# Kernel optimization log

Hardware: AMD Instinct MI355X
Metric: run time of the kernel (lower is better)

Reference implementation:

```python
import jax, jax.numpy as jnp
import numpy as np
from jax.scipy.stats import norm

B, IN, H0, H1, OUT = 1024, 2048, 4096, 4096, 1000
EPS_CDF = 1e-5
DECAY = 0.01
NEG_SLOPE = 0.01  # LeakyReLU default slope


def setup_inputs() -> dict:
    key = jax.random.key(0)
    ks = iter(jax.random.split(key, 40))
    rn = lambda shp, s=1.0: s * jax.random.normal(next(ks), shp, dtype=jnp.float32)
    inp = {}
    inp['x'] = rn((B, IN))
    inp['z_w'] = rn((IN,), 0.02)
    for nm, (o, i) in zip(['0', '1', 'o'], [(H0, IN), (H1, H0), (OUT, H1)]):
        inp['w_mu' + nm] = rn((o, i), 0.02)
        inp['w_ls' + nm] = rn((o, i), 0.1) - 2.0  # log-sigma ~ -2 => sigma ~ 0.13
        inp['b_mu' + nm] = rn((o,), 0.02)
        inp['b_ls' + nm] = rn((o,), 0.1) - 2.0
        inp['eps_w' + nm] = rn((o, i))
        inp['eps_b' + nm] = rn((o,))
    inp['pfz0'] = jax.random.uniform(next(ks), (B, H0), dtype=jnp.float32)
    inp['pfz1'] = jax.random.uniform(next(ks), (B, H1), dtype=jnp.float32)
    inp['y'] = jax.random.randint(next(ks), (B,), 0, OUT, dtype=jnp.int32)
    inp['mz0'] = jax.random.randint(next(ks), (B, H0), 0, 2, dtype=jnp.int32)
    inp['mz1'] = jax.random.randint(next(ks), (B, H1), 0, 2, dtype=jnp.int32)
    inp['mask_mu0'] = jax.random.randint(next(ks), (H0,), 0, 2, dtype=jnp.int32)
    inp['mask_mu1'] = jax.random.randint(next(ks), (H1,), 0, 2, dtype=jnp.int32)
    inp['data_set_size'] = 60000
    return inp


def _bayes_layer(h, w_mu, w_ls, b_mu, b_ls, eps_w, eps_b, mz, mask_mu, pfz):
    sw = jnp.exp(w_ls)
    sb = jnp.exp(b_ls)
    w = w_mu + sw * eps_w          # reparameterized weight sample
    b = b_mu + sb * eps_b
    h = h @ w.T + b                # F.linear
    h = jnp.where(h >= 0, h, NEG_SLOPE * h)  # LeakyReLU
    mzf = mz.astype(h.dtype)
    m = mzf * mask_mu.astype(h.dtype)[None, :]   # [B, h]
    mult = m.shape[1] / (m.sum(1) + 1e-6)        # rescale multiplier per sample
    h = h * m * mult[:, None]
    # GFN forward-flow log-prob of the z-mask
    p = jnp.clip(pfz, 1e-6, 1.0 - 1e-6)
    flow = (mzf * jnp.log(p) + (1.0 - mzf) * jnp.log(1.0 - p)).sum()
    # Gaussian CDF likelihood of sampled weights/biases (finite-difference density)
    pw = norm.cdf(w + EPS_CDF, w_mu, sw) - norm.cdf(w - EPS_CDF, w_mu, sw)
    pb = norm.cdf(b + EPS_CDF, b_mu, sb) - norm.cdf(b - EPS_CDF, b_mu, sb)
    flow = flow + jnp.log(pw).sum() + jnp.log(pb).sum()
    return h, flow


def reference(x, z_w, w_mu0, w_ls0, b_mu0, b_ls0, eps_w0, eps_b0,
              w_mu1, w_ls1, b_mu1, b_ls1, eps_w1, eps_b1,
              w_muo, w_lso, b_muo, b_lso, eps_wo, eps_bo,
              pfz0, pfz1, y, mz0, mz1, mask_mu0, mask_mu1, data_set_size):
    loss = (x @ z_w).sum()  # total flow estimator Z
    h, f0 = _bayes_layer(x, w_mu0, w_ls0, b_mu0, b_ls0, eps_w0, eps_b0, mz0, mask_mu0, pfz0)
    loss = loss + f0
    h, f1 = _bayes_layer(h, w_mu1, w_ls1, b_mu1, b_ls1, eps_w1, eps_b1, mz1, mask_mu1, pfz1)
    loss = loss + f1
    # output BayesLinear (sampled)
    wo = w_muo + jnp.exp(w_lso) * eps_wo
    bo = b_muo + jnp.exp(b_lso) * eps_bo
    pred = h @ wo.T + bo  # [B, OUT]
    logp = jax.nn.log_softmax(pred, axis=-1)
    ce = -jnp.take_along_axis(logp, y[:, None].astype(jnp.int32), axis=1).mean()
    loss = loss + jnp.float32(data_set_size) * ce  # NLL
    wd = DECAY * ((w_mu0 ** 2).sum() + jnp.exp(w_ls0).sum()
                  + (w_mu1 ** 2).sum() + jnp.exp(w_ls1).sum())
    loss = (loss + wd) ** 2
    return pred, loss
```

## Files before the change

kernel.cpp:

```cpp
#include <hip/hip_runtime.h>
#include <math.h>

#define B_SZ 1024
#define IN_SZ 2048
#define H0_SZ 4096
#define H1_SZ 4096
#define OUT_SZ 1000

typedef _Float16 f16;
typedef __attribute__((ext_vector_type(4))) _Float16 f16x4;
typedef __attribute__((ext_vector_type(8))) _Float16 f16x8;
typedef __attribute__((ext_vector_type(4))) float f32x4;

#define OFF_N0     0ULL
#define OFF_N1     4ULL
#define OFF_MSUM0  256ULL
#define OFF_MSUM1  4352ULL
#define OFF_CPOS0  8448ULL
#define OFF_CPOS1  24832ULL
#define OFF_IDX0   41216ULL
#define OFF_IDX1   57600ULL
#define OFF_PXZ    73984ULL
#define OFF_PFL    82176ULL
#define OFF_PCE    98560ULL
#define OFF_PB     106752ULL
#define OFF_PW     107776ULL
#define OFF_BS0    370688ULL
#define OFF_BS1    387072ULL
#define OFF_BSO    403456ULL
#define OFF_XH     407552ULL
#define OFF_XL     4601856ULL
#define OFF_H0H    8796160ULL
#define OFF_H0L    17184768ULL
#define OFF_H1H    25573376ULL
#define OFF_H1L    33961984ULL
#define OFF_W0CH   42350592ULL
#define OFF_W0CL   59127808ULL
#define OFF_W1CH   75905024ULL
#define OFF_W1CL   109459456ULL
#define OFF_WOCH   143013888ULL
#define OFF_WOCL   151402496ULL
#define OFF_PART   159791104ULL

#define PSTRIDE_H  2560
#define PSTRIDE_O  1024

#define RB_W1   4096
#define RB_WO   5096
#define RB_W0   9192
#define RB_FL0  10216
#define RB_FL1  11240
#define RB_SX   11496
#define RB_B0   11512
#define RB_B1   11528
#define RB_BO   11532

__device__ __forceinline__ void gload_lds16(const void* g, void* l)
{
    __builtin_amdgcn_global_load_lds((const __attribute__((address_space(1))) void*)g,
                                     (__attribute__((address_space(3))) void*)l, 16, 0, 0);
}

__device__ __forceinline__ void reduce4_store(double v0, double v1, double v2, double v3,
                                              double* dst)
{
    __shared__ double sh[4][4];
    double v[4] = {v0, v1, v2, v3};
    int lane = threadIdx.x & 63, wid = threadIdx.x >> 6;
#pragma unroll
    for (int a = 0; a < 4; ++a) {
        double x = v[a];
#pragma unroll
        for (int o = 32; o > 0; o >>= 1) x += __shfl_down(x, o, 64);
        if (lane == 0) sh[a][wid] = x;
    }
    __syncthreads();
    if (threadIdx.x == 0) {
        dst[0] = sh[0][0] + sh[0][1] + sh[0][2] + sh[0][3];
        dst[1] = sh[1][0] + sh[1][1] + sh[1][2] + sh[1][3];
        dst[2] = sh[2][0] + sh[2][1] + sh[2][2] + sh[2][3];
        dst[3] = sh[3][0] + sh[3][1] + sh[3][2] + sh[3][3];
    }
}

__device__ __forceinline__ void reduce1_store(double v, double* dst)
{
    __shared__ double sh1[4];
    int lane = threadIdx.x & 63, wid = threadIdx.x >> 6;
#pragma unroll
    for (int o = 32; o > 0; o >>= 1) v += __shfl_down(v, o, 64);
    if (lane == 0) sh1[wid] = v;
    __syncthreads();
    if (threadIdx.x == 0) dst[0] = sh1[0] + sh1[1] + sh1[2] + sh1[3];
}

__global__ __launch_bounds__(1024) void idxbuild_kernel(
    const int* __restrict__ mask0, const int* __restrict__ mask1,
    int* __restrict__ cpos0, int* __restrict__ idx0, int* __restrict__ n0,
    int* __restrict__ cpos1, int* __restrict__ idx1, int* __restrict__ n1)
{
    __shared__ int sh[1024];
    const int t = threadIdx.x;
    const int pass = blockIdx.x;
    const int* mask = pass ? mask1 : mask0;
    int* cpos = pass ? cpos1 : cpos0;
    int* idx = pass ? idx1 : idx0;
    int* np = pass ? n1 : n0;
    int4 m = ((const int4*)mask)[t];
    int s = m.x + m.y + m.z + m.w;
    sh[t] = s;
    __syncthreads();
    for (int o = 1; o < 1024; o <<= 1) {
        int v = (t >= o) ? sh[t - o] : 0;
        __syncthreads();
        sh[t] += v;
        __syncthreads();
    }
    int run = sh[t] - s;
    int4 cp;
    cp.x = run; cp.y = run + m.x; cp.z = cp.y + m.y; cp.w = cp.z + m.z;
    ((int4*)cpos)[t] = cp;
    if (m.x) idx[cp.x] = 4 * t + 0;
    if (m.y) idx[cp.y] = 4 * t + 1;
    if (m.z) idx[cp.z] = 4 * t + 2;
    if (m.w) idx[cp.w] = 4 * t + 3;
    if (t == 1023) *np = sh[1023];
}


__device__ void role_splitx(int rb, const float4* x, const float4* zw,
                            f16x4* xh, f16x4* xl, double* pxz)
{
    const int n4 = B_SZ * IN_SZ / 4;
    double s = 0;
    int i = rb * 256 + threadIdx.x;
    const int stride = 256 * 256;
    for (; i < n4; i += stride) {
        float4 v = x[i];
        float4 z = zw[i & (IN_SZ / 4 - 1)];
        s += (double)((v.x * z.x + v.y * z.y) + (v.z * z.z + v.w * z.w));
        f16 h0 = (f16)v.x, h1 = (f16)v.y, h2 = (f16)v.z, h3 = (f16)v.w;
        f16x4 hv = {h0, h1, h2, h3};
        f16x4 lv = {(f16)(v.x - (float)h0), (f16)(v.y - (float)h1),
                    (f16)(v.z - (float)h2), (f16)(v.w - (float)h3)};
        xh[i] = hv; xl[i] = lv;
    }
    reduce1_store(s, pxz + rb);
}

__device__ void role_flow(int b, const int* mz, const float* pfz, const int* maskmu,
                          float* msum, double* pfl)
{
    const int4* m4 = (const int4*)(mz + (size_t)b * 4096);
    const float4* p4 = (const float4*)(pfz + (size_t)b * 4096);
    const int4* k4 = (const int4*)maskmu;
    int s = 0;
    double fl = 0;
    for (int i = threadIdx.x; i < 1024; i += 256) {
        int4 m = m4[i];
        float4 p = p4[i];
        int4 k = k4[i];
        s += m.x * k.x + m.y * k.y + m.z * k.z + m.w * k.w;
        float a0 = fminf(fmaxf(p.x, 1e-6f), 1.0f - 1e-6f);
        float a1 = fminf(fmaxf(p.y, 1e-6f), 1.0f - 1e-6f);
        float a2 = fminf(fmaxf(p.z, 1e-6f), 1.0f - 1e-6f);
        float a3 = fminf(fmaxf(p.w, 1e-6f), 1.0f - 1e-6f);
        float g0 = logf(m.x ? a0 : 1.0f - a0);
        float g1 = logf(m.y ? a1 : 1.0f - a1);
        float g2 = logf(m.z ? a2 : 1.0f - a2);
        float g3 = logf(m.w ? a3 : 1.0f - a3);
        fl += (double)((g0 + g1) + (g2 + g3));
    }
#pragma unroll
    for (int o = 32; o > 0; o >>= 1) {
        s += __shfl_down(s, o, 64);
        fl += __shfl_down(fl, o, 64);
    }
    __shared__ int shi[4];
    __shared__ double shd[4];
    if ((threadIdx.x & 63) == 0) { shi[threadIdx.x >> 6] = s; shd[threadIdx.x >> 6] = fl; }
    __syncthreads();
    if (threadIdx.x == 0) {
        msum[b] = (float)(shi[0] + shi[1] + shi[2] + shi[3]);
        pfl[b] = shd[0] + shd[1] + shd[2] + shd[3];
    }
}

template <int RED>
__device__ void role_bsample(int rb, const float* bmu, const float* bls, const float* beps,
                             float* out, int n, double* pb)
{
    int i = rb * 256 + threadIdx.x;
    float l = 0.f, e = 0.f;
    if (i < n) {
        l = bls[i]; e = beps[i];
        out[i] = fmaf(__expf(l), e, bmu[i]);
    }
    if (RED) {
        double sls = (i < n) ? (double)l : 0.0;
        double se2 = (i < n) ? (double)e * e : 0.0;
        reduce4_store(sls, se2, 0.0, 0.0, pb + (size_t)rb * 4);
    }
}

__device__ void role_w0(int r, const float* mu, const float* ls, const float* eps,
                        const int* maskR, const int* cposR, f16* hi, double* pw)
{
    const size_t rbb = (size_t)r * IN_SZ;
    const float4* m4 = (const float4*)(mu + rbb);
    const float4* l4 = (const float4*)(ls + rbb);
    const float4* e4 = (const float4*)(eps + rbb);
    const bool wr_ = maskR[r] != 0;
    const int drow = cposR[r];
    f16* hrow = hi + (size_t)drow * IN_SZ;
    double sls = 0, se2 = 0, smu2 = 0, sex = 0;
    for (int i = threadIdx.x; i < IN_SZ / 4; i += 256) {
        float4 m = m4[i], l = l4[i], e = e4[i];
        float g0 = __expf(l.x), g1 = __expf(l.y), g2 = __expf(l.z), g3 = __expf(l.w);
        float w0 = fmaf(g0, e.x, m.x), w1 = fmaf(g1, e.y, m.y);
        float w2 = fmaf(g2, e.z, m.z), w3 = fmaf(g3, e.w, m.w);
        sls += (double)((l.x + l.y) + (l.z + l.w));
        se2 += (double)((e.x * e.x + e.y * e.y) + (e.z * e.z + e.w * e.w));
        smu2 += (double)((m.x * m.x + m.y * m.y) + (m.z * m.z + m.w * m.w));
        sex += (double)((g0 + g1) + (g2 + g3));
        if (wr_) {
            f16x4 hv = {(f16)w0, (f16)w1, (f16)w2, (f16)w3};
            *(f16x4*)(hrow + i * 4) = hv;
        }
    }
    reduce4_store(sls, se2, smu2, sex, pw + (size_t)r * 4);
}

__shared__ __align__(16) f16 g_ldsH[4096];

template <int ROWC, int RED>
__device__ void role_colc(int r, const float* mu, const float* ls, const float* eps,
                          const int* maskR, const int* cposR,
                          const int* maskC, const int* cposC, const int* pNc,
                          f16* hi, double* pw)
{
    const size_t rbb = (size_t)r * 4096;
    const float4* m4 = (const float4*)(mu + rbb);
    const float4* l4 = (const float4*)(ls + rbb);
    const float4* e4 = (const float4*)(eps + rbb);
    const bool wr_ = ROWC ? (maskR[r] != 0) : true;
    const int drow = ROWC ? cposR[r] : r;
    const int t = threadIdx.x;
    const f16x8 z8 = {0, 0, 0, 0, 0, 0, 0, 0};
    for (int i = t; i < 512; i += 256) ((f16x8*)g_ldsH)[i] = z8;
    __syncthreads();
    double sls = 0, se2 = 0, smu2 = 0, sex = 0;
    for (int i = t; i < 1024; i += 256) {
        float4 m = m4[i], l = l4[i], e = e4[i];
        float g0 = __expf(l.x), g1 = __expf(l.y), g2 = __expf(l.z), g3 = __expf(l.w);
        float w0 = fmaf(g0, e.x, m.x), w1 = fmaf(g1, e.y, m.y);
        float w2 = fmaf(g2, e.z, m.z), w3 = fmaf(g3, e.w, m.w);
        if (RED) {
            sls += (double)((l.x + l.y) + (l.z + l.w));
            se2 += (double)((e.x * e.x + e.y * e.y) + (e.z * e.z + e.w * e.w));
            smu2 += (double)((m.x * m.x + m.y * m.y) + (m.z * m.z + m.w * m.w));
            sex += (double)((g0 + g1) + (g2 + g3));
        }
        if (wr_) {
            int4 mc = ((const int4*)maskC)[i];
            int4 cp = ((const int4*)cposC)[i];
            if (mc.x) g_ldsH[cp.x] = (f16)w0;
            if (mc.y) g_ldsH[cp.y] = (f16)w1;
            if (mc.z) g_ldsH[cp.z] = (f16)w2;
            if (mc.w) g_ldsH[cp.w] = (f16)w3;
        }
    }
    __syncthreads();
    if (wr_) {
        const int n8 = ((*pNc + 127) >> 7) << 4;
        f16x8* hd = (f16x8*)(hi + (size_t)drow * 4096);
        for (int i = t; i < n8; i += 256) hd[i] = ((const f16x8*)g_ldsH)[i];
    }
    if (RED) reduce4_store(sls, se2, smu2, sex, pw + (size_t)r * 4);
}

__global__ __launch_bounds__(256) void prep_kernel(
    const float* __restrict__ x, const float* __restrict__ zw,
    const float* __restrict__ wmu0, const float* __restrict__ wls0, const float* __restrict__ weps0,
    const float* __restrict__ bmu0, const float* __restrict__ bls0, const float* __restrict__ beps0,
    const float* __restrict__ wmu1, const float* __restrict__ wls1, const float* __restrict__ weps1,
    const float* __restrict__ bmu1, const float* __restrict__ bls1, const float* __restrict__ beps1,
    const float* __restrict__ wmuo, const float* __restrict__ wlso, const float* __restrict__ wepso,
    const float* __restrict__ bmuo, const float* __restrict__ blso, const float* __restrict__ bepso,
    const float* __restrict__ pfz0, const float* __restrict__ pfz1,
    const int* __restrict__ mz0, const int* __restrict__ mz1,
    const int* __restrict__ mmu0, const int* __restrict__ mmu1,
    const int* __restrict__ cpos0, const int* __restrict__ cpos1,
    const int* __restrict__ n0p, const int* __restrict__ n1p,
    f16* __restrict__ xh, f16* __restrict__ xl,
    f16* __restrict__ w0ch, f16* __restrict__ w1ch, f16* __restrict__ woch,
    float* __restrict__ bs0, float* __restrict__ bs1, float* __restrict__ bso,
    float* __restrict__ msum0, float* __restrict__ msum1,
    double* __restrict__ PXZ, double* __restrict__ PFL,
    double* __restrict__ PB, double* __restrict__ PW)
{
    const int b = blockIdx.x;
    if (b < RB_W1) {
        role_colc<1, 1>(b, wmu1, wls1, weps1, mmu1, cpos1, mmu0, cpos0, n0p,
                        w1ch, PW + (size_t)4096 * 4);
    } else if (b < RB_WO) {
        role_colc<0, 0>(b - RB_W1, wmuo, wlso, wepso, nullptr, nullptr, mmu1, cpos1, n1p,
                        woch, nullptr);
    } else if (b < RB_W0) {
        role_w0(b - RB_WO, wmu0, wls0, weps0, mmu0, cpos0, w0ch, PW);
    } else if (b < RB_FL0) {
        role_flow(b - RB_W0, mz0, pfz0, mmu0, msum0, PFL);
    } else if (b < RB_FL1) {
        role_flow(b - RB_FL0, mz1, pfz1, mmu1, msum1, PFL + 1024);
    } else if (b < RB_SX) {
        role_splitx(b - RB_FL1, (const float4*)x, (const float4*)zw,
                    (f16x4*)xh, (f16x4*)xl, PXZ);
    } else if (b < RB_B0) {
        role_bsample<1>(b - RB_SX, bmu0, bls0, beps0, bs0, H0_SZ, PB);
    } else if (b < RB_B1) {
        role_bsample<1>(b - RB_B0, bmu1, bls1, beps1, bs1, H1_SZ, PB + 16 * 4);
    } else {
        role_bsample<0>(b - RB_B1, bmuo, blso, bepso, bso, OUT_SZ, nullptr);
    }
}

template <int NSPLIT>
__global__ __launch_bounds__(256, 3) void mg128b(
    const f16* __restrict__ Ah, const f16* __restrict__ Al, int SA,
    const f16* __restrict__ Wh, int SW,
    const int* __restrict__ pN, int NFIX,
    const int* __restrict__ pK, int KFIX,
    float* __restrict__ P0, float* __restrict__ P1,
    float* __restrict__ P2, float* __restrict__ P3,
    float* __restrict__ P4, float* __restrict__ P5,
    float* __restrict__ P6, float* __restrict__ P7, int pstride)
{
    const int bid = blockIdx.x;
    const int c8 = bid & 7, j = bid >> 3;
    int nt, mt, z;
    if (NSPLIT == 4) {
        const int p = c8 + 8 * (j % 10);
        nt = p >> 2; z = p & 3; mt = j / 10;
    } else {
        const int p = c8 + 8 * (j & 7);
        nt = p >> 3; z = p & 7; mt = j >> 3;
    }
    const int nvalid = pN ? *pN : NFIX;
    const int bn = nt * 128;
    if (bn >= nvalid) return;
    const int bm = mt * 128;
    const int kvalid = pK ? *pK : KFIX;
    const int ktiles = (kvalid + 31) >> 5;
    const int prt = (ktiles + NSPLIT - 1) / NSPLIT;
    const int kt0 = z * prt;
    const int kt1 = min(ktiles, kt0 + prt);
    float* Cf = (z == 0) ? P0 : (z == 1) ? P1 : (z == 2) ? P2 : (z == 3) ? P3
              : (z == 4) ? P4 : (z == 5) ? P5 : (z == 6) ? P6 : P7;

    __shared__ __align__(16) f16 lds[2][12288];
    const int tid = threadIdx.x;
    const int wv = tid >> 6, lane = tid & 63;
    const int wr = wv >> 1, wc = wv & 1;
    const int l15 = lane & 15, l4 = lane >> 4;

    const f16* sg[6];
    int ldst[6];
#pragma unroll
    for (int i = 0; i < 6; ++i) {
        const int c = wv * 6 + i;
        const int plane = c >> 3, cidx = c & 7;
        const f16* base = (plane == 0) ? Ah : (plane == 1) ? Al : Wh;
        const int S_ = (plane < 2) ? SA : SW;
        const int rowb = (plane < 2) ? bm : bn;
        sg[i] = base + (size_t)(rowb + cidx * 16 + l15) * S_ + l4 * 8;
        ldst[i] = c * 512 + lane * 8;
    }

#define STAGE(KT, B) do { \
        _Pragma("unroll") \
        for (int i_ = 0; i_ < 6; ++i_) \
            gload_lds16(sg[i_] + (size_t)(KT) * 32, &lds[B][ldst[i_]]); \
    } while (0)

    f32x4 acc[4][4];
#pragma unroll
    for (int m = 0; m < 4; ++m)
#pragma unroll
        for (int n = 0; n < 4; ++n) acc[m][n] = (f32x4){0.f, 0.f, 0.f, 0.f};

    if (kt0 < kt1) {
        STAGE(kt0, 0);
        int cur = 0;
        for (int kt = kt0; kt < kt1; ++kt) {
            asm volatile("s_waitcnt vmcnt(0)" ::: "memory");
            __builtin_amdgcn_s_barrier();
            __builtin_amdgcn_sched_barrier(0);
            if (kt + 1 < kt1) STAGE(kt + 1, cur ^ 1);
            __builtin_amdgcn_sched_barrier(0);
            const f16* L = &lds[cur][0];
            f16x8 ah[4], al[4], wh[4];
#pragma unroll
            for (int m = 0; m < 4; ++m) {
                ah[m] = *(const f16x8*)(L + (wr * 4 + m) * 512 + lane * 8);
                al[m] = *(const f16x8*)(L + 4096 + (wr * 4 + m) * 512 + lane * 8);
            }
#pragma unroll
            for (int n = 0; n < 4; ++n)
                wh[n] = *(const f16x8*)(L + 8192 + (wc * 4 + n) * 512 + lane * 8);
#pragma unroll
            for (int m = 0; m < 4; ++m)
#pragma unroll
                for (int n = 0; n < 4; ++n)
                    acc[m][n] = __builtin_amdgcn_mfma_f32_16x16x32_f16(ah[m], wh[n], acc[m][n], 0, 0, 0);
#pragma unroll
            for (int m = 0; m < 4; ++m)
#pragma unroll
                for (int n = 0; n < 4; ++n)
                    acc[m][n] = __builtin_amdgcn_mfma_f32_16x16x32_f16(al[m], wh[n], acc[m][n], 0, 0, 0);
            cur ^= 1;
        }
    }
#undef STAGE

#pragma unroll
    for (int n = 0; n < 4; ++n) {
        const int c = bn + wc * 64 + n * 16 + l15;
        if (c >= pstride) continue;
#pragma unroll
        for (int m = 0; m < 4; ++m)
#pragma unroll
            for (int j2 = 0; j2 < 4; ++j2) {
                const int row = bm + wr * 64 + m * 16 + l4 * 4 + j2;
                Cf[(size_t)row * pstride + c] = acc[m][n][j2];
            }
    }
}

__global__ __launch_bounds__(256) void combine4_kernel(
    const float* __restrict__ PA, const float* __restrict__ PB,
    const float* __restrict__ PC, const float* __restrict__ PD, int pstride,
    const float* __restrict__ bsamp, const int* __restrict__ idx,
    const int* __restrict__ mz, const float* __restrict__ msum,
    const int* __restrict__ pN,
    f16* __restrict__ Chh, f16* __restrict__ Chl)
{
    const int nv = *pN;
    const int bn = blockIdx.x * 64;
    const int bm = blockIdx.y * 64;
    const int t = threadIdx.x;
    const int c0 = bn + (t & 15) * 4;
    const int r0 = bm + (t >> 4);
#pragma unroll
    for (int rr = 0; rr < 4; ++rr) {
        const int row = r0 + rr * 16;
        const float mult = 4096.0f / (msum[row] + 1e-6f);
        float sv[4] = {0.f, 0.f, 0.f, 0.f};
        if (c0 < pstride) {
            float4 a = *(const float4*)(PA + (size_t)row * pstride + c0);
            float4 b = *(const float4*)(PB + (size_t)row * pstride + c0);
            float4 c = *(const float4*)(PC + (size_t)row * pstride + c0);
            float4 d = *(const float4*)(PD + (size_t)row * pstride + c0);
            sv[0] = (a.x + b.x) + (c.x + d.x);
            sv[1] = (a.y + b.y) + (c.y + d.y);
            sv[2] = (a.z + b.z) + (c.z + d.z);
            sv[3] = (a.w + b.w) + (c.w + d.w);
        }
        f16 hh[4], ll[4];
#pragma unroll
        for (int jj = 0; jj < 4; ++jj) {
            const int c = c0 + jj;
            float v = 0.f;
            if (c < nv) {
                const int orig = idx[c];
                v = sv[jj] + bsamp[orig];
                v = v >= 0.f ? v : 0.01f * v;
                v = v * (float)mz[(size_t)row * 4096 + orig] * mult;
            }
            hh[jj] = (f16)v;
            ll[jj] = (f16)(v - (float)hh[jj]);
        }
        f16x4 hv = {hh[0], hh[1], hh[2], hh[3]};
        f16x4 lv = {ll[0], ll[1], ll[2], ll[3]};
        *(f16x4*)(Chh + (size_t)row * 4096 + c0) = hv;
        *(f16x4*)(Chl + (size_t)row * 4096 + c0) = lv;
    }
}

__global__ __launch_bounds__(256) void ce_fused8_kernel(
    const float* __restrict__ Q0, const float* __restrict__ Q1,
    const float* __restrict__ Q2, const float* __restrict__ Q3,
    const float* __restrict__ Q4, const float* __restrict__ Q5,
    const float* __restrict__ Q6, const float* __restrict__ Q7,
    const float* __restrict__ bso, const int* __restrict__ y,
    float* __restrict__ pred, double* __restrict__ pce)
{
    const int b = blockIdx.x;
    float mx = -1e30f;
    for (int jj = threadIdx.x; jj < OUT_SZ; jj += 256) {
        const size_t o = (size_t)b * PSTRIDE_O + jj;
        float v = ((Q0[o] + Q1[o]) + (Q2[o] + Q3[o]))
                + ((Q4[o] + Q5[o]) + (Q6[o] + Q7[o])) + bso[jj];
        pred[(size_t)b * OUT_SZ + jj] = v;
        mx = fmaxf(mx, v);
    }
#pragma unroll
    for (int o = 32; o > 0; o >>= 1) mx = fmaxf(mx, __shfl_down(mx, o, 64));
    __shared__ float sm[4];
    if ((threadIdx.x & 63) == 0) sm[threadIdx.x >> 6] = mx;
    __syncthreads();
    mx = fmaxf(fmaxf(sm[0], sm[1]), fmaxf(sm[2], sm[3]));
    double se = 0;
    for (int jj = threadIdx.x; jj < OUT_SZ; jj += 256)
        se += (double)__expf(pred[(size_t)b * OUT_SZ + jj] - mx);
#pragma unroll
    for (int o = 32; o > 0; o >>= 1) se += __shfl_down(se, o, 64);
    __shared__ double sd[4];
    if ((threadIdx.x & 63) == 0) sd[threadIdx.x >> 6] = se;
    __syncthreads();
    if (threadIdx.x == 0) {
        double lse = (double)mx + log(sd[0] + sd[1] + sd[2] + sd[3]);
        pce[b] = lse - (double)pred[(size_t)b * OUT_SZ + y[b]];
    }
}

__global__ __launch_bounds__(256) void finalize_kernel(
    const double* __restrict__ PXZ, const double* __restrict__ PFL,
    const double* __restrict__ PCE, const double* __restrict__ PB,
    const double* __restrict__ PW, const int* __restrict__ dss, float* __restrict__ out)
{
    const int t = threadIdx.x;
    double xz = 0, fl = 0, ce = 0, ls = 0, e2 = 0, mu2 = 0, ex = 0;
    if (t < 256) { if (t < 256) xz += PXZ[t]; }
    for (int i = t; i < 2048; i += 256) fl += PFL[i];
    for (int i = t; i < 1024; i += 256) ce += PCE[i];
    for (int i = t; i < 8192; i += 256) {
        const double* p = PW + (size_t)i * 4;
        ls += p[0]; e2 += p[1]; mu2 += p[2]; ex += p[3];
    }
    if (t < 32) { ls += PB[t * 4]; e2 += PB[t * 4 + 1]; }
    __shared__ double sh[7][4];
    double v[7] = {xz, fl, ce, ls, e2, mu2, ex};
    const int lane = t & 63, wid = t >> 6;
#pragma unroll
    for (int a = 0; a < 7; ++a) {
        double x = v[a];
#pragma unroll
        for (int o = 32; o > 0; o >>= 1) x += __shfl_down(x, o, 64);
        if (lane == 0) sh[a][wid] = x;
    }
    __syncthreads();
    if (t == 0) {
        double T[7];
#pragma unroll
        for (int a = 0; a < 7; ++a) T[a] = sh[a][0] + sh[a][1] + sh[a][2] + sh[a][3];
        const double NTOT = 25174016.0;
        double cst = NTOT * (log(2.0e-5) - 0.91893853320467274178);
        double loss = T[0]
                    + cst - T[3] - 0.5 * T[4]
                    + T[1]
                    + (double)(*dss) * (T[2] / (double)B_SZ)
                    + 0.01 * (T[5] + T[6]);
        out[(size_t)B_SZ * OUT_SZ] = (float)(loss * loss);
    }
}

extern "C" void kernel_launch(void* const* d_in, const int* in_sizes, int n_in,
                              void* d_out, int out_size, void* d_ws, size_t ws_size,
                              hipStream_t stream)
{
    const float* x = (const float*)d_in[0];
    const float* zw = (const float*)d_in[1];
    const float* wmu0 = (const float*)d_in[2];
    const float* wls0 = (const float*)d_in[3];
    const float* bmu0 = (const float*)d_in[4];
    const float* bls0 = (const float*)d_in[5];
    const float* weps0 = (const float*)d_in[6];
    const float* beps0 = (const float*)d_in[7];
    const float* wmu1 = (const float*)d_in[8];
    const float* wls1 = (const float*)d_in[9];
    const float* bmu1 = (const float*)d_in[10];
    const float* bls1 = (const float*)d_in[11];
    const float* weps1 = (const float*)d_in[12];
    const float* beps1 = (const float*)d_in[13];
    const float* wmuo = (const float*)d_in[14];
    const float* wlso = (const float*)d_in[15];
    const float* bmuo = (const float*)d_in[16];
    const float* blso = (const float*)d_in[17];
    const float* wepso = (const float*)d_in[18];
    const float* bepso = (const float*)d_in[19];
    const float* pfz0 = (const float*)d_in[20];
    const float* pfz1 = (const float*)d_in[21];
    const int* y = (const int*)d_in[22];
    const int* mz0 = (const int*)d_in[23];
    const int* mz1 = (const int*)d_in[24];
    const int* mmu0 = (const int*)d_in[25];
    const int* mmu1 = (const int*)d_in[26];
    const int* dss = (const int*)d_in[27];

    char* ws = (char*)d_ws;
    int* n0p = (int*)(ws + OFF_N0);
    int* n1p = (int*)(ws + OFF_N1);
    float* msum0 = (float*)(ws + OFF_MSUM0);
    float* msum1 = (float*)(ws + OFF_MSUM1);
    int* cpos0 = (int*)(ws + OFF_CPOS0);
    int* cpos1 = (int*)(ws + OFF_CPOS1);
    int* idx0 = (int*)(ws + OFF_IDX0);
    int* idx1 = (int*)(ws + OFF_IDX1);
    double* PXZ = (double*)(ws + OFF_PXZ);
    double* PFL = (double*)(ws + OFF_PFL);
    double* PCE = (double*)(ws + OFF_PCE);
    double* PB = (double*)(ws + OFF_PB);
    double* PW = (double*)(ws + OFF_PW);
    float* bs0 = (float*)(ws + OFF_BS0);
    float* bs1 = (float*)(ws + OFF_BS1);
    float* bso = (float*)(ws + OFF_BSO);
    f16* xh = (f16*)(ws + OFF_XH);
    f16* xl = (f16*)(ws + OFF_XL);
    f16* h0h = (f16*)(ws + OFF_H0H);
    f16* h0l = (f16*)(ws + OFF_H0L);
    f16* h1h = (f16*)(ws + OFF_H1H);
    f16* h1l = (f16*)(ws + OFF_H1L);
    f16* w0ch = (f16*)(ws + OFF_W0CH);
    f16* w1ch = (f16*)(ws + OFF_W1CH);
    f16* woch = (f16*)(ws + OFF_WOCH);
    float* out = (float*)d_out;

    float* A0 = (float*)(ws + OFF_H1H);
    float* A1 = (float*)(ws + OFF_PART);
    float* A2 = (float*)(ws + OFF_W0CL);
    float* A3 = (float*)(ws + OFF_W1CL);
    float* B0 = (float*)(ws + OFF_W0CH);
    float* B1 = (float*)(ws + OFF_W0CL);
    float* B2 = (float*)(ws + OFF_W1CL);
    float* B3 = (float*)(ws + OFF_PART);
    float* Q[8];
    for (int i = 0; i < 8; ++i) Q[i] = (float*)(ws + OFF_W0CH + (size_t)i * 4194304ULL);

    idxbuild_kernel<<<2, 1024, 0, stream>>>(mmu0, mmu1, cpos0, idx0, n0p, cpos1, idx1, n1p);

    prep_kernel<<<RB_BO, 256, 0, stream>>>(
        x, zw, wmu0, wls0, weps0, bmu0, bls0, beps0,
        wmu1, wls1, weps1, bmu1, bls1, beps1,
        wmuo, wlso, wepso, bmuo, blso, bepso,
        pfz0, pfz1, mz0, mz1, mmu0, mmu1, cpos0, cpos1, n0p, n1p,
        xh, xl, w0ch, w1ch, woch, bs0, bs1, bso, msum0, msum1,
        PXZ, PFL, PB, PW);

    mg128b<4><<<640, 256, 0, stream>>>(
        xh, xl, IN_SZ, w0ch, IN_SZ, n0p, 0, nullptr, IN_SZ,
        A0, A1, A2, A3, nullptr, nullptr, nullptr, nullptr, PSTRIDE_H);
    combine4_kernel<<<dim3(64, 16), 256, 0, stream>>>(
        A0, A1, A2, A3, PSTRIDE_H, bs0, idx0, mz0, msum0, n0p, h0h, h0l);
    mg128b<4><<<640, 256, 0, stream>>>(
        h0h, h0l, 4096, w1ch, 4096, n1p, 0, n0p, 0,
        B0, B1, B2, B3, nullptr, nullptr, nullptr, nullptr, PSTRIDE_H);
    combine4_kernel<<<dim3(64, 16), 256, 0, stream>>>(
        B0, B1, B2, B3, PSTRIDE_H, bs1, idx1, mz1, msum1, n1p, h1h, h1l);
    mg128b<8><<<512, 256, 0, stream>>>(
        h1h, h1l, 4096, woch, 4096, nullptr, OUT_SZ, n1p, 0,
        Q[0], Q[1], Q[2], Q[3], Q[4], Q[5], Q[6], Q[7], PSTRIDE_O);

    ce_fused8_kernel<<<B_SZ, 256, 0, stream>>>(Q[0], Q[1], Q[2], Q[3], Q[4], Q[5], Q[6], Q[7],
                                               bso, y, out, PCE);
    finalize_kernel<<<1, 256, 0, stream>>>(PXZ, PFL, PCE, PB, PW, dss, out);
}
```

Baseline: 271.7 us.

## Split prep kernel and co-schedule weight sampling with preceding GEMM launches

The single prep kernel is split up. Layer-0 sampling stays in a smaller prepA kernel. Layer-1 weight sampling, flow and bias work become extra blocks of the layer-0 GEMM launch, and output-layer weight sampling becomes extra blocks of the layer-1 GEMM launch. The aim is to overlap this memory-bound sampling with compute-bound GEMM blocks and cut the serialized prep phase. In exchange, the sampling blocks now run under the GEMM's launch bounds and larger LDS allocation, which may lower their occupancy and contend for bandwidth with the GEMMs.

```diff
diff --git a/kernel.cpp b/kernel.cpp
--- a/kernel.cpp
+++ b/kernel.cpp
@@ -45,15 +45,17 @@
 #define PSTRIDE_H  2560
 #define PSTRIDE_O  1024
 
-#define RB_W1   4096
-#define RB_WO   5096
-#define RB_W0   9192
-#define RB_FL0  10216
-#define RB_FL1  11240
-#define RB_SX   11496
-#define RB_B0   11512
-#define RB_B1   11528
-#define RB_BO   11532
+#define PA_W0   4096
+#define PA_FL0  5120
+#define PA_SX   5376
+#define PA_B0   5392
+#define L0_G    640
+#define L0_W1   4736
+#define L0_FL1  5760
+#define L0_B1   5776
+#define L1_G    640
+#define L1_WO   1640
+#define L1_BO   1644
 
 __device__ __forceinline__ void gload_lds16(const void* g, void* l)
 {
@@ -231,13 +233,11 @@
     reduce4_store(sls, se2, smu2, sex, pw + (size_t)r * 4);
 }
 
-__shared__ __align__(16) f16 g_ldsH[4096];
-
 template <int ROWC, int RED>
 __device__ void role_colc(int r, const float* mu, const float* ls, const float* eps,
                           const int* maskR, const int* cposR,
                           const int* maskC, const int* cposC, const int* pNc,
-                          f16* hi, double* pw)
+                          f16* hi, double* pw, f16* ldsH)
 {
     const size_t rbb = (size_t)r * 4096;
     const float4* m4 = (const float4*)(mu + rbb);
@@ -247,7 +247,7 @@
     const int drow = ROWC ? cposR[r] : r;
     const int t = threadIdx.x;
     const f16x8 z8 = {0, 0, 0, 0, 0, 0, 0, 0};
-    for (int i = t; i < 512; i += 256) ((f16x8*)g_ldsH)[i] = z8;
+    for (int i = t; i < 512; i += 256) ((f16x8*)ldsH)[i] = z8;
     __syncthreads();
     double sls = 0, se2 = 0, smu2 = 0, sex = 0;
     for (int i = t; i < 1024; i += 256) {
@@ -264,78 +264,29 @@
         if (wr_) {
             int4 mc = ((const int4*)maskC)[i];
             int4 cp = ((const int4*)cposC)[i];
-            if (mc.x) g_ldsH[cp.x] = (f16)w0;
-            if (mc.y) g_ldsH[cp.y] = (f16)w1;
-            if (mc.z) g_ldsH[cp.z] = (f16)w2;
-            if (mc.w) g_ldsH[cp.w] = (f16)w3;
+            if (mc.x) ldsH[cp.x] = (f16)w0;
+            if (mc.y) ldsH[cp.y] = (f16)w1;
+            if (mc.z) ldsH[cp.z] = (f16)w2;
+            if (mc.w) ldsH[cp.w] = (f16)w3;
         }
     }
     __syncthreads();
     if (wr_) {
         const int n8 = ((*pNc + 127) >> 7) << 4;
         f16x8* hd = (f16x8*)(hi + (size_t)drow * 4096);
-        for (int i = t; i < n8; i += 256) hd[i] = ((const f16x8*)g_ldsH)[i];
+        for (int i = t; i < n8; i += 256) hd[i] = ((const f16x8*)ldsH)[i];
     }
     if (RED) reduce4_store(sls, se2, smu2, sex, pw + (size_t)r * 4);
 }
 
-__global__ __launch_bounds__(256) void prep_kernel(
-    const float* __restrict__ x, const float* __restrict__ zw,
-    const float* __restrict__ wmu0, const float* __restrict__ wls0, const float* __restrict__ weps0,
-    const float* __restrict__ bmu0, const float* __restrict__ bls0, const float* __restrict__ beps0,
-    const float* __restrict__ wmu1, const float* __restrict__ wls1, const float* __restrict__ weps1,
-    const float* __restrict__ bmu1, const float* __restrict__ bls1, const float* __restrict__ beps1,
-    const float* __restrict__ wmuo, const float* __restrict__ wlso, const float* __restrict__ wepso,
-    const float* __restrict__ bmuo, const float* __restrict__ blso, const float* __restrict__ bepso,
-    const float* __restrict__ pfz0, const float* __restrict__ pfz1,
-    const int* __restrict__ mz0, const int* __restrict__ mz1,
-    const int* __restrict__ mmu0, const int* __restrict__ mmu1,
-    const int* __restrict__ cpos0, const int* __restrict__ cpos1,
-    const int* __restrict__ n0p, const int* __restrict__ n1p,
-    f16* __restrict__ xh, f16* __restrict__ xl,
-    f16* __restrict__ w0ch, f16* __restrict__ w1ch, f16* __restrict__ woch,
-    float* __restrict__ bs0, float* __restrict__ bs1, float* __restrict__ bso,
-    float* __restrict__ msum0, float* __restrict__ msum1,
-    double* __restrict__ PXZ, double* __restrict__ PFL,
-    double* __restrict__ PB, double* __restrict__ PW)
-{
-    const int b = blockIdx.x;
-    if (b < RB_W1) {
-        role_colc<1, 1>(b, wmu1, wls1, weps1, mmu1, cpos1, mmu0, cpos0, n0p,
-                        w1ch, PW + (size_t)4096 * 4);
-    } else if (b < RB_WO) {
-        role_colc<0, 0>(b - RB_W1, wmuo, wlso, wepso, nullptr, nullptr, mmu1, cpos1, n1p,
-                        woch, nullptr);
-    } else if (b < RB_W0) {
-        role_w0(b - RB_WO, wmu0, wls0, weps0, mmu0, cpos0, w0ch, PW);
-    } else if (b < RB_FL0) {
-        role_flow(b - RB_W0, mz0, pfz0, mmu0, msum0, PFL);
-    } else if (b < RB_FL1) {
-        role_flow(b - RB_FL0, mz1, pfz1, mmu1, msum1, PFL + 1024);
-    } else if (b < RB_SX) {
-        role_splitx(b - RB_FL1, (const float4*)x, (const float4*)zw,
-                    (f16x4*)xh, (f16x4*)xl, PXZ);
-    } else if (b < RB_B0) {
-        role_bsample<1>(b - RB_SX, bmu0, bls0, beps0, bs0, H0_SZ, PB);
-    } else if (b < RB_B1) {
-        role_bsample<1>(b - RB_B0, bmu1, bls1, beps1, bs1, H1_SZ, PB + 16 * 4);
-    } else {
-        role_bsample<0>(b - RB_B1, bmuo, blso, bepso, bso, OUT_SZ, nullptr);
-    }
-}
-
 template <int NSPLIT>
-__global__ __launch_bounds__(256, 3) void mg128b(
-    const f16* __restrict__ Ah, const f16* __restrict__ Al, int SA,
-    const f16* __restrict__ Wh, int SW,
-    const int* __restrict__ pN, int NFIX,
-    const int* __restrict__ pK, int KFIX,
-    float* __restrict__ P0, float* __restrict__ P1,
-    float* __restrict__ P2, float* __restrict__ P3,
-    float* __restrict__ P4, float* __restrict__ P5,
-    float* __restrict__ P6, float* __restrict__ P7, int pstride)
-{
-    const int bid = blockIdx.x;
+__device__ void gemm_body(int bid, f16* ldsbase,
+                          const f16* Ah, const f16* Al, int SA,
+                          const f16* Wh, int SW,
+                          const int* pN, int NFIX, const int* pK, int KFIX,
+                          float* P0, float* P1, float* P2, float* P3,
+                          float* P4, float* P5, float* P6, float* P7, int pstride)
+{
     const int c8 = bid & 7, j = bid >> 3;
     int nt, mt, z;
     if (NSPLIT == 4) {
@@ -357,7 +308,6 @@
     float* Cf = (z == 0) ? P0 : (z == 1) ? P1 : (z == 2) ? P2 : (z == 3) ? P3
               : (z == 4) ? P4 : (z == 5) ? P5 : (z == 6) ? P6 : P7;
 
-    __shared__ __align__(16) f16 lds[2][12288];
     const int tid = threadIdx.x;
     const int wv = tid >> 6, lane = tid & 63;
     const int wr = wv >> 1, wc = wv & 1;
@@ -379,7 +329,7 @@
 #define STAGE(KT, B) do { \
         _Pragma("unroll") \
         for (int i_ = 0; i_ < 6; ++i_) \
-            gload_lds16(sg[i_] + (size_t)(KT) * 32, &lds[B][ldst[i_]]); \
+            gload_lds16(sg[i_] + (size_t)(KT) * 32, ldsbase + (B) * 12288 + ldst[i_]); \
     } while (0)
 
     f32x4 acc[4][4];
@@ -397,7 +347,7 @@
             __builtin_amdgcn_sched_barrier(0);
             if (kt + 1 < kt1) STAGE(kt + 1, cur ^ 1);
             __builtin_amdgcn_sched_barrier(0);
-            const f16* L = &lds[cur][0];
+            const f16* L = ldsbase + cur * 12288;
             f16x8 ah[4], al[4], wh[4];
 #pragma unroll
             for (int m = 0; m < 4; ++m) {
@@ -434,6 +384,92 @@
                 Cf[(size_t)row * pstride + c] = acc[m][n][j2];
             }
     }
+}
+
+__global__ __launch_bounds__(256) void prepA_kernel(
+    const float* __restrict__ x, const float* __restrict__ zw,
+    const float* __restrict__ wmu0, const float* __restrict__ wls0, const float* __restrict__ weps0,
+    const float* __restrict__ bmu0, const float* __restrict__ bls0, const float* __restrict__ beps0,
+    const float* __restrict__ pfz0, const int* __restrict__ mz0,
+    const int* __restrict__ mmu0, const int* __restrict__ cpos0,
+    f16* __restrict__ xh, f16* __restrict__ xl, f16* __restrict__ w0ch,
+    float* __restrict__ bs0, float* __restrict__ msum0,
+    double* __restrict__ PXZ, double* __restrict__ PFL,
+    double* __restrict__ PB, double* __restrict__ PW)
+{
+    const int b = blockIdx.x;
+    if (b < PA_W0) {
+        role_w0(b, wmu0, wls0, weps0, mmu0, cpos0, w0ch, PW);
+    } else if (b < PA_FL0) {
+        role_flow(b - PA_W0, mz0, pfz0, mmu0, msum0, PFL);
+    } else if (b < PA_SX) {
+        role_splitx(b - PA_FL0, (const float4*)x, (const float4*)zw,
+                    (f16x4*)xh, (f16x4*)xl, PXZ);
+    } else {
+        role_bsample<1>(b - PA_SX, bmu0, bls0, beps0, bs0, H0_SZ, PB);
+    }
+}
+
+__global__ __launch_bounds__(256, 3) void gemmL0_kernel(
+    const f16* __restrict__ xh, const f16* __restrict__ xl, const f16* __restrict__ w0ch,
+    const int* __restrict__ n0p,
+    float* __restrict__ A0, float* __restrict__ A1,
+    float* __restrict__ A2, float* __restrict__ A3,
+    const float* __restrict__ wmu1, const float* __restrict__ wls1, const float* __restrict__ weps1,
+    const float* __restrict__ bmu1, const float* __restrict__ bls1, const float* __restrict__ beps1,
+    const float* __restrict__ pfz1, const int* __restrict__ mz1,
+    const int* __restrict__ mmu0, const int* __restrict__ mmu1,
+    const int* __restrict__ cpos0, const int* __restrict__ cpos1,
+    f16* __restrict__ w1ch, float* __restrict__ bs1, float* __restrict__ msum1,
+    double* __restrict__ PFL, double* __restrict__ PB, double* __restrict__ PW)
+{
+    __shared__ __align__(16) f16 lds[2][12288];
+    const int b = blockIdx.x;
+    if (b < L0_G) {
+        gemm_body<4>(b, &lds[0][0], xh, xl, IN_SZ, w0ch, IN_SZ, n0p, 0, nullptr, IN_SZ,
+                     A0, A1, A2, A3, nullptr, nullptr, nullptr, nullptr, PSTRIDE_H);
+    } else if (b < L0_W1) {
+        role_colc<1, 1>(b - L0_G, wmu1, wls1, weps1, mmu1, cpos1, mmu0, cpos0, n0p,
+                        w1ch, PW + (size_t)4096 * 4, &lds[0][0]);
+    } else if (b < L0_FL1) {
+        role_flow(b - L0_W1, mz1, pfz1, mmu1, msum1, PFL + 1024);
+    } else {
+        role_bsample<1>(b - L0_FL1, bmu1, bls1, beps1, bs1, H1_SZ, PB + 16 * 4);
+    }
+}
+
+__global__ __launch_bounds__(256, 3) void gemmL1_kernel(
+    const f16* __restrict__ h0h, const f16* __restrict__ h0l, const f16* __restrict__ w1ch,
+    const int* __restrict__ n1p, const int* __restrict__ n0p,
+    float* __restrict__ B0, float* __restrict__ B1,
+    float* __restrict__ B2, float* __restrict__ B3,
+    const float* __restrict__ wmuo, const float* __restrict__ wlso, const float* __restrict__ wepso,
+    const float* __restrict__ bmuo, const float* __restrict__ blso, const float* __restrict__ bepso,
+    const int* __restrict__ mmu1, const int* __restrict__ cpos1,
+    f16* __restrict__ woch, float* __restrict__ bso)
+{
+    __shared__ __align__(16) f16 lds[2][12288];
+    const int b = blockIdx.x;
+    if (b < L1_G) {
+        gemm_body<4>(b, &lds[0][0], h0h, h0l, 4096, w1ch, 4096, n1p, 0, n0p, 0,
+                     B0, B1, B2, B3, nullptr, nullptr, nullptr, nullptr, PSTRIDE_H);
+    } else if (b < L1_WO) {
+        role_colc<0, 0>(b - L1_G, wmuo, wlso, wepso, nullptr, nullptr, mmu1, cpos1, n1p,
+                        woch, nullptr, &lds[0][0]);
+    } else {
+        role_bsample<0>(b - L1_WO, bmuo, blso, bepso, bso, OUT_SZ, nullptr);
+    }
+}
+
+__global__ __launch_bounds__(256, 3) void gemmLo_kernel(
+    const f16* __restrict__ h1h, const f16* __restrict__ h1l, const f16* __restrict__ woch,
+    const int* __restrict__ n1p,
+    float* __restrict__ Q0, float* __restrict__ Q1, float* __restrict__ Q2, float* __restrict__ Q3,
+    float* __restrict__ Q4, float* __restrict__ Q5, float* __restrict__ Q6, float* __restrict__ Q7)
+{
+    __shared__ __align__(16) f16 lds[2][12288];
+    gemm_body<8>(blockIdx.x, &lds[0][0], h1h, h1l, 4096, woch, 4096, nullptr, OUT_SZ, n1p, 0,
+                 Q0, Q1, Q2, Q3, Q4, Q5, Q6, Q7, PSTRIDE_O);
 }
 
 __global__ __launch_bounds__(256) void combine4_kernel(
@@ -530,7 +566,7 @@
 {
     const int t = threadIdx.x;
     double xz = 0, fl = 0, ce = 0, ls = 0, e2 = 0, mu2 = 0, ex = 0;
-    if (t < 256) { if (t < 256) xz += PXZ[t]; }
+    xz += PXZ[t];
     for (int i = t; i < 2048; i += 256) fl += PFL[i];
     for (int i = t; i < 1024; i += 256) ce += PCE[i];
     for (int i = t; i < 8192; i += 256) {
@@ -638,27 +674,28 @@
 
     idxbuild_kernel<<<2, 1024, 0, stream>>>(mmu0, mmu1, cpos0, idx0, n0p, cpos1, idx1, n1p);
 
-    prep_kernel<<<RB_BO, 256, 0, stream>>>(
+    prepA_kernel<<<PA_B0, 256, 0, stream>>>(
         x, zw, wmu0, wls0, weps0, bmu0, bls0, beps0,
+        pfz0, mz0, mmu0, cpos0,
+        xh, xl, w0ch, bs0, msum0, PXZ, PFL, PB, PW);
+
+    gemmL0_kernel<<<L0_B1, 256, 0, stream>>>(
+        xh, xl, w0ch, n0p, A0, A1, A2, A3,
         wmu1, wls1, weps1, bmu1, bls1, beps1,
-        wmuo, wlso, wepso, bmuo, blso, bepso,
-        pfz0, pfz1, mz0, mz1, mmu0, mmu1, cpos0, cpos1, n0p, n1p,
-        xh, xl, w0ch, w1ch, woch, bs0, bs1, bso, msum0, msum1,
-        PXZ, PFL, PB, PW);
-
-    mg128b<4><<<640, 256, 0, stream>>>(
-        xh, xl, IN_SZ, w0ch, IN_SZ, n0p, 0, nullptr, IN_SZ,
-        A0, A1, A2, A3, nullptr, nullptr, nullptr, nullptr, PSTRIDE_H);
+        pfz1, mz1, mmu0, mmu1, cpos0, cpos1,
+        w1ch, bs1, msum1, PFL, PB, PW);
     combine4_kernel<<<dim3(64, 16), 256, 0, stream>>>(
         A0, A1, A2, A3, PSTRIDE_H, bs0, idx0, mz0, msum0, n0p, h0h, h0l);
-    mg128b<4><<<640, 256, 0, stream>>>(
-        h0h, h0l, 4096, w1ch, 4096, n1p, 0, n0p, 0,
-        B0, B1, B2, B3, nullptr, nullptr, nullptr, nullptr, PSTRIDE_H);
+
+    gemmL1_kernel<<<L1_BO, 256, 0, stream>>>(
+        h0h, h0l, w1ch, n1p, n0p, B0, B1, B2, B3,
+        wmuo, wlso, wepso, bmuo, blso, bepso,
+        mmu1, cpos1, woch, bso);
     combine4_kernel<<<dim3(64, 16), 256, 0, stream>>>(
         B0, B1, B2, B3, PSTRIDE_H, bs1, idx1, mz1, msum1, n1p, h1h, h1l);
-    mg128b<8><<<512, 256, 0, stream>>>(
-        h1h, h1l, 4096, woch, 4096, nullptr, OUT_SZ, n1p, 0,
-        Q[0], Q[1], Q[2], Q[3], Q[4], Q[5], Q[6], Q[7], PSTRIDE_O);
+
+    gemmLo_kernel<<<512, 256, 0, stream>>>(
+        h1h, h1l, woch, n1p, Q[0], Q[1], Q[2], Q[3], Q[4], Q[5], Q[6], Q[7]);
 
     ce_fused8_kernel<<<B_SZ, 256, 0, stream>>>(Q[0], Q[1], Q[2], Q[3], Q[4], Q[5], Q[6], Q[7],
                                                bso, y, out, PCE);
```

Result: faster. 256.0 us (-5.8%).
